# Performance work log

Hardware: AMD Instinct MI355X
Metric: run time of the kernel (lower is better)

## Reference

```python
import jax, jax.numpy as jnp
import numpy as np

N = 50000
E = 800000
D = 128          # feature_dimension
H = 2 * D        # hidden = 2*feature_dimension
C = 8            # num_edge_colours


def setup_inputs() -> dict:
    key = jax.random.key(0)
    ks = jax.random.split(key, 9)
    x = jax.random.normal(ks[0], (N, D), dtype=jnp.float32)
    edge_index = jax.random.randint(ks[1], (2, E), 0, N, dtype=jnp.int64)
    edge_colour = jax.random.randint(ks[2], (E,), 0, C, dtype=jnp.int64)
    # conv weights init: normal(0, 0.001) as in the torch module
    W_conv1 = 0.001 * jax.random.normal(ks[3], (C, H, D), dtype=jnp.float32)
    W_conv2 = 0.001 * jax.random.normal(ks[4], (C, D, H), dtype=jnp.float32)
    # nn.Linear default init: U(-1/sqrt(fan_in), 1/sqrt(fan_in))
    b1 = 1.0 / np.sqrt(D)
    b2 = 1.0 / np.sqrt(H)
    W_self1 = jax.random.uniform(ks[5], (H, D), jnp.float32, -b1, b1)
    b_self1 = jax.random.uniform(ks[6], (H,), jnp.float32, -b1, b1)
    W_self2 = jax.random.uniform(ks[7], (D, H), jnp.float32, -b2, b2)
    b_self2 = jax.random.uniform(ks[8], (D,), jnp.float32, -b2, b2)
    return {
        "x": x, "edge_index": edge_index, "edge_colour": edge_colour,
        "W_self1": W_self1, "b_self1": b_self1,
        "W_self2": W_self2, "b_self2": b_self2,
        "W_conv1": W_conv1, "W_conv2": W_conv2,
    }


def _ec_conv(h, src, seg, Wc):
    # Per-colour gather -> scatter-add -> colour-specific linear, summed over colours.
    # seg = colour * N + dst combines (colour, dst) into one segment id so a single
    # segment_sum covers all colours (equivalent to the per-colour masked loops).
    msgs = h[src]                                             # [E, F]
    agg = jax.ops.segment_sum(msgs, seg, num_segments=C * N)  # [C*N, F]
    agg = agg.reshape(C, N, h.shape[1])                       # [C, N, F]
    return jnp.einsum('cnf,cof->no', agg, Wc)                 # [N, O]


def reference(x, edge_index, edge_colour, W_self1, b_self1, W_self2, b_self2,
              W_conv1, W_conv2):
    src = edge_index[0]   # message() uses x_j = x[src], aggregated at dst
    dst = edge_index[1]
    seg = edge_colour * N + dst
    h = x @ W_self1.T + b_self1 + _ec_conv(x, src, seg, W_conv1)
    h = jax.nn.relu(h)
    h2 = h @ W_self2.T + b_self2 + _ec_conv(h, src, seg, W_conv2)
    return jax.nn.sigmoid(h2 - 10.0)
```

## Files before the change

### kernel.cpp

```cpp
#include <hip/hip_runtime.h>


#define NN 50000
#define EE 800000
#define DD 128
#define HH 256
#define CC 8
#define K1 1152

typedef unsigned short u16;
typedef __attribute__((ext_vector_type(8))) short s16x8;
typedef __attribute__((ext_vector_type(4))) float f32x4;

__device__ __forceinline__ float bf2f(short u) {
  return __uint_as_float(((unsigned)(u16)u) << 16);
}
__device__ __forceinline__ u16 f2bf(float f) {
  unsigned u = __float_as_uint(f);
  u = (u + 0x7FFFu + ((u >> 16) & 1u)) >> 16;
  return (u16)u;
}


__global__ void k_castx(const float* __restrict__ x, u16* __restrict__ xb) {
  int i = blockIdx.x * 256 + threadIdx.x;
  if (i < NN * DD) xb[i] = f2bf(x[i]);
}

__global__ void k_wt1f(const float* __restrict__ Wc1, const float* __restrict__ Ws1,
                       u16* __restrict__ W) {
  int i = blockIdx.x * 256 + threadIdx.x;
  if (i >= 294912) return;
  int e = i & 7;
  int t = i >> 3;
  int rs = t & 15; t >>= 4;
  int kg = t & 3;  t >>= 2;
  int kk = t % 36;
  int col16 = t / 36;
  int col = col16 * 16 + rs;
  int k = kk * 32 + kg * 8 + e;
  float v = (k < CC * DD) ? Wc1[(k >> 7) * (HH * DD) + col * DD + (k & 127)]
                          : Ws1[col * DD + (k - CC * DD)];
  W[i] = f2bf(v);
}

__global__ void k_wt2f(const float* __restrict__ Wc2, const float* __restrict__ Ws2,
                       u16* __restrict__ W) {
  int i = blockIdx.x * 256 + threadIdx.x;
  if (i >= 294912) return;
  int e = i & 7;
  int t = i >> 3;
  int rs = t & 15; t >>= 4;
  int kg = t & 3;  t >>= 2;
  int kk = t & 7;
  int col16 = t >> 3;
  int oc = col16 * 16 + rs;
  int c = oc >> 7, o = oc & 127;
  int k = kk * 32 + kg * 8 + e;
  float v = (c < CC) ? Wc2[c * (DD * HH) + o * HH + k] : Ws2[o * HH + k];
  W[i] = f2bf(v);
}


__global__ void k_hist(const int* __restrict__ ei, const int* __restrict__ ec,
                       int* __restrict__ counts) {
  int e = blockIdx.x * 256 + threadIdx.x;
  if (e < EE) {
    int dst = ei[EE + e];
    int c = ec[e];
    atomicAdd(&counts[dst * CC + c], 1);
  }
}

__global__ void k_offsets(const int* __restrict__ counts, int2* __restrict__ oc,
                          int* __restrict__ cursor, int* __restrict__ gcount) {
  __shared__ int lds[256];
  __shared__ int basesh;
  int tid = threadIdx.x;
  int i = blockIdx.x * 256 + tid;
  int c = (i < CC * NN) ? counts[i] : 0;
  lds[tid] = c;
  __syncthreads();
  int v = c;
  for (int s = 1; s < 256; s <<= 1) {
    int t = (tid >= s) ? lds[tid - s] : 0;
    __syncthreads();
    v += t;
    lds[tid] = v;
    __syncthreads();
  }
  if (tid == 255) basesh = atomicAdd(gcount, v);
  __syncthreads();
  int excl = basesh + v - c;
  if (i < CC * NN) {
    oc[i] = make_int2(excl, c);
    cursor[i] = excl;
  }
}

__global__ void k_fill(const int* __restrict__ ei, const int* __restrict__ ec,
                       int* __restrict__ cursor, int* __restrict__ sv) {
  int e = blockIdx.x * 256 + threadIdx.x;
  if (e < EE) {
    int src = ei[e];
    int dst = ei[EE + e];
    int c = ec[e];
    int slot = atomicAdd(&cursor[dst * CC + c], 1);
    sv[slot] = src * 8 + c;
  }
}


__global__ void __launch_bounds__(256) k_agg1(
    const u16* __restrict__ xb, const int2* __restrict__ oc,
    const int* __restrict__ sv, u16* __restrict__ agg) {
  int item = blockIdx.x * 256 + threadIdx.x;
  int dst = item >> 4, ch = item & 15;
  int eoff = ch * 8;
#pragma unroll
  for (int c = 0; c < CC; ++c) {
    int2 se = oc[dst * CC + c];
    float s[8];
#pragma unroll
    for (int q = 0; q < 8; q++) s[q] = 0.f;
    int j = 0;
    for (; j + 1 < se.y; j += 2) {
      int s0 = sv[se.x + j] >> 3;
      int s1 = sv[se.x + j + 1] >> 3;
      s16x8 v0 = *(const s16x8*)(xb + (size_t)s0 * DD + eoff);
      s16x8 v1 = *(const s16x8*)(xb + (size_t)s1 * DD + eoff);
#pragma unroll
      for (int q = 0; q < 8; q++) s[q] += bf2f(v0[q]) + bf2f(v1[q]);
    }
    if (j < se.y) {
      int s0 = sv[se.x + j] >> 3;
      s16x8 v0 = *(const s16x8*)(xb + (size_t)s0 * DD + eoff);
#pragma unroll
      for (int q = 0; q < 8; q++) s[q] += bf2f(v0[q]);
    }
    s16x8 r;
#pragma unroll
    for (int q = 0; q < 8; q++) r[q] = (short)f2bf(s[q]);
    *(s16x8*)(agg + ((size_t)c * NN + dst) * DD + eoff) = r;
  }
}


#define LOADA(af, p) do {                                                      \
  if ((p) < CC) {                                                              \
    _Pragma("unroll") for (int rg = 0; rg < 2; ++rg)                           \
    _Pragma("unroll") for (int kk = 0; kk < 4; ++kk)                           \
      af[rg][kk] = *(const s16x8*)(agg + ((size_t)(p) * NN + rowA[rg]) * DD +  \
                                   kk * 32 + kg * 8);                          \
  } else {                                                                     \
    _Pragma("unroll") for (int rg = 0; rg < 2; ++rg)                           \
    _Pragma("unroll") for (int kk = 0; kk < 4; ++kk)                           \
      af[rg][kk] = *(const s16x8*)(xb + (size_t)rowA[rg] * DD +                \
                                   kk * 32 + kg * 8);                          \
  } } while (0)

#define STAGE1(p, buf) do {                                                    \
  _Pragma("unroll") for (int i = 0; i < 8; ++i) {                              \
    const u16* gsrc = Wf + (size_t)((ch * 8 + i) * 36 + (p) * 4 + w) * 512 +   \
                      lane * 8;                                                \
    u16* lptr = Bs + (buf) * 16384 + (i * 4 + w) * 512;                        \
    __builtin_amdgcn_global_load_lds(                                          \
        (const __attribute__((address_space(1))) void*)gsrc,                   \
        (__attribute__((address_space(3))) void*)lptr, 16, 0, 0);              \
  } } while (0)

#define MFMAPH(af, buf) do {                                                   \
  _Pragma("unroll") for (int kk = 0; kk < 4; ++kk)                             \
  _Pragma("unroll") for (int fc = 0; fc < 8; ++fc) {                           \
    s16x8 bfr = *(const s16x8*)(Bs + (buf) * 16384 + (fc * 4 + kk) * 512 +     \
                                lane * 8);                                     \
    _Pragma("unroll") for (int rg = 0; rg < 2; ++rg)                           \
      acc[rg][fc] = __builtin_amdgcn_mfma_f32_16x16x32_bf16(af[rg][kk], bfr,   \
                                                            acc[rg][fc], 0, 0, 0); \
  } } while (0)

__global__ void __launch_bounds__(256, 1) k_gemm1s(
    const u16* __restrict__ xb, const u16* __restrict__ agg,
    const u16* __restrict__ Wf, const float* __restrict__ b1,
    u16* __restrict__ hb) {
  __shared__ u16 Bs[32768];
  int ch = blockIdx.x;
  int rb = blockIdx.y;
  int tid = threadIdx.x;
  int w = tid >> 6, lane = tid & 63;
  int rs = lane & 15, kg = lane >> 4;
  int r0 = rb * 128 + w * 32;

  int rowA[2];
#pragma unroll
  for (int rg = 0; rg < 2; ++rg) rowA[rg] = min(r0 + rg * 16 + rs, NN - 1);

  f32x4 acc[2][8];
#pragma unroll
  for (int rg = 0; rg < 2; ++rg)
#pragma unroll
    for (int i = 0; i < 8; i++)
#pragma unroll
      for (int q = 0; q < 4; q++) acc[rg][i][q] = 0.f;

  s16x8 afA[2][4], afB[2][4];
  STAGE1(0, 0);
  LOADA(afA, 0);
  __syncthreads();

#pragma unroll
  for (int ph = 0; ph < 9; ++ph) {
    const int pb = ph & 1;
    if (ph < 8) {
      STAGE1(ph + 1, pb ^ 1);
      if (pb == 0) { LOADA(afB, ph + 1); } else { LOADA(afA, ph + 1); }
    }
    if (pb == 0) { MFMAPH(afA, 0); } else { MFMAPH(afB, 1); }
    __syncthreads();
  }

#pragma unroll
  for (int fc = 0; fc < 8; ++fc) {
    int col = ch * 128 + fc * 16 + rs;
    float bias = b1[col];
#pragma unroll
    for (int rg = 0; rg < 2; ++rg) {
#pragma unroll
      for (int q = 0; q < 4; ++q) {
        float v = acc[rg][fc][q] + bias;
        if (v < 0.f) v = 0.f;
        int rr = r0 + rg * 16 + kg * 4 + q;
        if (rr < NN) hb[(size_t)rr * HH + col] = f2bf(v);
      }
    }
  }
}


__global__ void __launch_bounds__(256, 3) k_gemm2g(
    const u16* __restrict__ hb, const u16* __restrict__ Wf,
    u16* __restrict__ g2) {
  __shared__ u16 Bs[24576];
  int cb = blockIdx.x;
  int rb = blockIdx.y;
  int tid = threadIdx.x;
  int w = tid >> 6, lane = tid & 63;
  int rs = lane & 15, kg = lane >> 4;
  int c16b = cb * 6;

  {
    const u16* src = Wf + (size_t)cb * 24576;
#pragma unroll
    for (int i = 0; i < 12; ++i) {
      int o = (i * 256 + tid) * 8;
      *(s16x8*)(Bs + o) = *(const s16x8*)(src + o);
    }
  }
  __syncthreads();

#pragma unroll
  for (int tt = 0; tt < 2; ++tt) {
    int t = w + tt * 4;
    int r0 = rb * 256 + t * 32;
    int rowA[2];
#pragma unroll
    for (int rg = 0; rg < 2; ++rg) rowA[rg] = min(r0 + rg * 16 + rs, NN - 1);

    s16x8 af[2][8];
#pragma unroll
    for (int rg = 0; rg < 2; ++rg)
#pragma unroll
      for (int kk = 0; kk < 8; ++kk)
        af[rg][kk] = *(const s16x8*)(hb + (size_t)rowA[rg] * HH + kk * 32 + kg * 8);

    f32x4 acc[2][6];
#pragma unroll
    for (int rg = 0; rg < 2; ++rg)
#pragma unroll
      for (int i = 0; i < 6; i++)
#pragma unroll
        for (int q = 0; q < 4; q++) acc[rg][i][q] = 0.f;

#pragma unroll
    for (int kk = 0; kk < 8; ++kk) {
#pragma unroll
      for (int fc = 0; fc < 6; ++fc) {
        s16x8 bfr = *(const s16x8*)(Bs + ((fc * 8 + kk) * 64 + lane) * 8);
#pragma unroll
        for (int rg = 0; rg < 2; ++rg)
          acc[rg][fc] = __builtin_amdgcn_mfma_f32_16x16x32_bf16(af[rg][kk], bfr, acc[rg][fc], 0, 0, 0);
      }
    }

#pragma unroll
    for (int rg = 0; rg < 2; ++rg) {
#pragma unroll
      for (int q = 0; q < 4; ++q) {
        int rr = r0 + rg * 16 + kg * 4 + q;
        if (rr < NN) {
#pragma unroll
          for (int fc = 0; fc < 6; ++fc) {
            int col = (c16b + fc) * 16 + rs;
            g2[(size_t)rr * 1152 + col] = f2bf(acc[rg][fc][q]);
          }
        }
      }
    }
  }
}


__global__ void __launch_bounds__(256) k_final(
    const u16* __restrict__ g2, const float* __restrict__ b2,
    const int2* __restrict__ oc, const int* __restrict__ sv,
    float* __restrict__ out) {
  int item = blockIdx.x * 256 + threadIdx.x;
  if (item >= NN * 8) return;
  int dst = item >> 3, ch = item & 7;
  int eoff = ch * 16;

  int st, cn;
  {
    int2 a0 = oc[dst * CC];
    int2 a7 = oc[dst * CC + 7];
    st = a0.x;
    cn = a7.x + a7.y - a0.x;
  }

  float s[16];
  {
    const u16* sp = g2 + (size_t)dst * 1152 + 1024 + eoff;
    s16x8 lo = *(const s16x8*)sp;
    s16x8 hi = *(const s16x8*)(sp + 8);
#pragma unroll
    for (int q = 0; q < 8; q++) s[q] = b2[eoff + q] + bf2f(lo[q]);
#pragma unroll
    for (int q = 0; q < 8; q++) s[q + 8] = b2[eoff + 8 + q] + bf2f(hi[q]);
  }

  for (int j = 0; j < cn; j += 4) {
    int pofs[4];
#pragma unroll
    for (int t = 0; t < 4; t++) {
      int jj = j + t;
      if (jj < cn) {
        int v = sv[st + jj];
        pofs[t] = (v >> 3) * 1152 + (v & 7) * 128;
      } else {
        pofs[t] = -1;
      }
    }
#pragma unroll
    for (int t = 0; t < 4; t++) {
      if (pofs[t] >= 0) {
        const u16* pp = g2 + pofs[t] + eoff;
        s16x8 lo = *(const s16x8*)pp;
        s16x8 hi = *(const s16x8*)(pp + 8);
#pragma unroll
        for (int q = 0; q < 8; q++) s[q] += bf2f(lo[q]);
#pragma unroll
        for (int q = 0; q < 8; q++) s[q + 8] += bf2f(hi[q]);
      }
    }
  }
  float* op = out + (size_t)dst * DD + eoff;
#pragma unroll
  for (int q = 0; q < 16; q++) op[q] = 1.f / (1.f + expf(10.f - s[q]));
}


extern "C" void kernel_launch(void* const* d_in, const int* in_sizes, int n_in,
                              void* d_out, int out_size, void* d_ws, size_t ws_size,
                              hipStream_t stream) {
  const float* x   = (const float*)d_in[0];
  const int*   ei  = (const int*)d_in[1];
  const int*   ec  = (const int*)d_in[2];
  const float* Ws1 = (const float*)d_in[3];
  const float* b1  = (const float*)d_in[4];
  const float* Ws2 = (const float*)d_in[5];
  const float* b2  = (const float*)d_in[6];
  const float* Wc1 = (const float*)d_in[7];
  const float* Wc2 = (const float*)d_in[8];
  float* out = (float*)d_out;

  char* p = (char*)d_ws;
  u16*  g2     = (u16*)p;
  u16*  agg1   = (u16*)p;
  u16*  xb     = (u16*)(p + 102400000);
  u16*  hb     = (u16*)(p + 115200000);
  u16*  W1f    = (u16*)(p + 140800000);
  u16*  W2f    = (u16*)(p + 141389824);
  int2* oc     = (int2*)(p + 141979648);
  int*  sv     = (int*)(p + 145179648);
  int*  counts = (int*)(p + 148379648);
  int*  gcount = (int*)(p + 149979648);
  int*  cursor = (int*)(p + 149979904);

  hipMemsetAsync(counts, 0, 1600256, stream);

  k_castx<<<25000, 256, 0, stream>>>(x, xb);
  k_wt1f<<<1152, 256, 0, stream>>>(Wc1, Ws1, W1f);
  k_wt2f<<<1152, 256, 0, stream>>>(Wc2, Ws2, W2f);

  k_hist<<<3125, 256, 0, stream>>>(ei, ec, counts);
  k_offsets<<<1563, 256, 0, stream>>>(counts, oc, cursor, gcount);
  k_fill<<<3125, 256, 0, stream>>>(ei, ec, cursor, sv);

  k_agg1<<<3125, 256, 0, stream>>>(xb, oc, sv, agg1);
  k_gemm1s<<<dim3(2, 391), 256, 0, stream>>>(xb, agg1, W1f, b1, hb);
  k_gemm2g<<<dim3(12, 196), 256, 0, stream>>>(hb, W2f, g2);
  k_final<<<1563, 256, 0, stream>>>(g2, b2, oc, sv, out);
}
```

Measured before the change: 350.2 us.

## Store layer-1 aggregates and conv weights in FP8 and use FP8 MFMA

The per-colour aggregates from k_agg1 are now written as FP8 (e4m3) instead of bf16. The layer-1 conv weights are pre-scaled by 256 and packed to FP8, and the first GEMM runs its eight colour phases with the fp8 MFMA, rescaling before a final bf16 phase for the self-weight term. This halves the aggregate write and read traffic and the weight staging bytes, and uses the higher-rate fp8 matrix instructions. It also vectorises the x-to-bf16 cast. The cost is reduced precision on aggregates and weights, with some risk to accuracy.

```diff
diff --git a/kernel.cpp b/kernel.cpp
--- a/kernel.cpp
+++ b/kernel.cpp
@@ -6,9 +6,10 @@
 #define DD 128
 #define HH 256
 #define CC 8
-#define K1 1152
 
 typedef unsigned short u16;
+typedef unsigned char u8;
+typedef unsigned long long u64;
 typedef __attribute__((ext_vector_type(8))) short s16x8;
 typedef __attribute__((ext_vector_type(4))) float f32x4;
 
@@ -24,24 +25,42 @@
 
 __global__ void k_castx(const float* __restrict__ x, u16* __restrict__ xb) {
   int i = blockIdx.x * 256 + threadIdx.x;
-  if (i < NN * DD) xb[i] = f2bf(x[i]);
-}
-
-__global__ void k_wt1f(const float* __restrict__ Wc1, const float* __restrict__ Ws1,
-                       u16* __restrict__ W) {
+  const float4* xp = (const float4*)x + (size_t)i * 2;
+  float4 a = xp[0], b = xp[1];
+  s16x8 r;
+  r[0] = f2bf(a.x); r[1] = f2bf(a.y); r[2] = f2bf(a.z); r[3] = f2bf(a.w);
+  r[4] = f2bf(b.x); r[5] = f2bf(b.y); r[6] = f2bf(b.z); r[7] = f2bf(b.w);
+  *(s16x8*)(xb + (size_t)i * 8) = r;
+}
+
+__global__ void k_wt1c8(const float* __restrict__ Wc1, unsigned* __restrict__ W) {
+  int t = blockIdx.x * 256 + threadIdx.x;
+  if (t >= 65536) return;
+  int half = t & 1;
+  int slot = t >> 1;
+  int lane = slot & 63;
+  int sk = slot >> 6;
+  int kkg = sk & 31, col16 = sk >> 5;
+  int col = col16 * 16 + (lane & 15);
+  int kb = kkg * 32 + (lane >> 4) * 8 + half * 4;
+  int c = kb >> 7, f = kb & 127;
+  const float* wp = Wc1 + (size_t)c * (HH * DD) + col * DD + f;
+  unsigned r = __builtin_amdgcn_cvt_pk_fp8_f32(wp[0] * 256.f, wp[1] * 256.f, 0, false);
+  r = __builtin_amdgcn_cvt_pk_fp8_f32(wp[2] * 256.f, wp[3] * 256.f, r, true);
+  W[t] = r;
+}
+
+__global__ void k_wt1s(const float* __restrict__ Ws1, u16* __restrict__ W) {
   int i = blockIdx.x * 256 + threadIdx.x;
-  if (i >= 294912) return;
+  if (i >= 32768) return;
   int e = i & 7;
-  int t = i >> 3;
-  int rs = t & 15; t >>= 4;
-  int kg = t & 3;  t >>= 2;
-  int kk = t % 36;
-  int col16 = t / 36;
-  int col = col16 * 16 + rs;
-  int k = kk * 32 + kg * 8 + e;
-  float v = (k < CC * DD) ? Wc1[(k >> 7) * (HH * DD) + col * DD + (k & 127)]
-                          : Ws1[col * DD + (k - CC * DD)];
-  W[i] = f2bf(v);
+  int slot = i >> 3;
+  int lane = slot & 63;
+  int sk = slot >> 6;
+  int kk = sk & 3, col16 = sk >> 2;
+  int col = col16 * 16 + (lane & 15);
+  int k = kk * 32 + (lane >> 4) * 8 + e;
+  W[i] = f2bf(Ws1[col * DD + k]);
 }
 
 __global__ void k_wt2f(const float* __restrict__ Wc2, const float* __restrict__ Ws2,
@@ -113,7 +132,7 @@
 
 __global__ void __launch_bounds__(256) k_agg1(
     const u16* __restrict__ xb, const int2* __restrict__ oc,
-    const int* __restrict__ sv, u16* __restrict__ agg) {
+    const int* __restrict__ sv, u8* __restrict__ aggf8) {
   int item = blockIdx.x * 256 + threadIdx.x;
   int dst = item >> 4, ch = item & 15;
   int eoff = ch * 8;
@@ -138,52 +157,75 @@
 #pragma unroll
       for (int q = 0; q < 8; q++) s[q] += bf2f(v0[q]);
     }
-    s16x8 r;
-#pragma unroll
-    for (int q = 0; q < 8; q++) r[q] = (short)f2bf(s[q]);
-    *(s16x8*)(agg + ((size_t)c * NN + dst) * DD + eoff) = r;
-  }
-}
-
-
-#define LOADA(af, p) do {                                                      \
-  if ((p) < CC) {                                                              \
-    _Pragma("unroll") for (int rg = 0; rg < 2; ++rg)                           \
-    _Pragma("unroll") for (int kk = 0; kk < 4; ++kk)                           \
-      af[rg][kk] = *(const s16x8*)(agg + ((size_t)(p) * NN + rowA[rg]) * DD +  \
-                                   kk * 32 + kg * 8);                          \
-  } else {                                                                     \
-    _Pragma("unroll") for (int rg = 0; rg < 2; ++rg)                           \
-    _Pragma("unroll") for (int kk = 0; kk < 4; ++kk)                           \
-      af[rg][kk] = *(const s16x8*)(xb + (size_t)rowA[rg] * DD +                \
-                                   kk * 32 + kg * 8);                          \
+    unsigned r0 = __builtin_amdgcn_cvt_pk_fp8_f32(s[0], s[1], 0, false);
+    r0 = __builtin_amdgcn_cvt_pk_fp8_f32(s[2], s[3], r0, true);
+    unsigned r1 = __builtin_amdgcn_cvt_pk_fp8_f32(s[4], s[5], 0, false);
+    r1 = __builtin_amdgcn_cvt_pk_fp8_f32(s[6], s[7], r1, true);
+    *(uint2*)(aggf8 + ((size_t)c * NN + dst) * 128 + eoff) = make_uint2(r0, r1);
+  }
+}
+
+
+#define LOADA8(af, p) do {                                                     \
+  _Pragma("unroll") for (int rg = 0; rg < 2; ++rg)                             \
+  _Pragma("unroll") for (int kk = 0; kk < 4; ++kk)                             \
+    af[rg][kk] = *(const u64*)(aggf8 + ((size_t)(p) * NN + rowA[rg]) * 128 +   \
+                               kk * 32 + kg * 8);                              \
+  } while (0)
+
+#define LOADAS(af) do {                                                        \
+  _Pragma("unroll") for (int rg = 0; rg < 2; ++rg)                             \
+  _Pragma("unroll") for (int kk = 0; kk < 4; ++kk)                             \
+    af[rg][kk] = *(const s16x8*)(xb + (size_t)rowA[rg] * DD + kk * 32 + kg * 8); \
+  } while (0)
+
+#define STAGE8(p, buf) do {                                                    \
+  _Pragma("unroll") for (int i2 = 0; i2 < 4; ++i2) {                           \
+    int fc = i2 * 2 + (w >> 1);                                                \
+    int kb2 = (w & 1) * 2;                                                     \
+    const char* gs = (const char*)W1c8 +                                       \
+        (((ch * 8 + fc) * 32 + (p) * 4 + kb2) << 9) + lane * 16;               \
+    char* lp = Bs + (buf) * 32768 + ((fc * 4 + kb2) << 9);                     \
+    __builtin_amdgcn_global_load_lds(                                          \
+        (const __attribute__((address_space(1))) void*)gs,                     \
+        (__attribute__((address_space(3))) void*)lp, 16, 0, 0);                \
   } } while (0)
 
-#define STAGE1(p, buf) do {                                                    \
-  _Pragma("unroll") for (int i = 0; i < 8; ++i) {                              \
-    const u16* gsrc = Wf + (size_t)((ch * 8 + i) * 36 + (p) * 4 + w) * 512 +   \
-                      lane * 8;                                                \
-    u16* lptr = Bs + (buf) * 16384 + (i * 4 + w) * 512;                        \
+#define STAGES(buf) do {                                                       \
+  _Pragma("unroll") for (int i2 = 0; i2 < 8; ++i2) {                           \
+    const char* gs = (const char*)W1s + (((ch * 8 + i2) * 4 + w) << 10) +      \
+                     lane * 16;                                                \
+    char* lp = Bs + (buf) * 32768 + ((i2 * 4 + w) << 10);                      \
     __builtin_amdgcn_global_load_lds(                                          \
-        (const __attribute__((address_space(1))) void*)gsrc,                   \
-        (__attribute__((address_space(3))) void*)lptr, 16, 0, 0);              \
+        (const __attribute__((address_space(1))) void*)gs,                     \
+        (__attribute__((address_space(3))) void*)lp, 16, 0, 0);                \
   } } while (0)
 
-#define MFMAPH(af, buf) do {                                                   \
+#define MFMA8(af, buf) do {                                                    \
   _Pragma("unroll") for (int kk = 0; kk < 4; ++kk)                             \
   _Pragma("unroll") for (int fc = 0; fc < 8; ++fc) {                           \
-    s16x8 bfr = *(const s16x8*)(Bs + (buf) * 16384 + (fc * 4 + kk) * 512 +     \
-                                lane * 8);                                     \
+    long bfr = *(const long*)(Bs + (buf) * 32768 + ((fc * 4 + kk) << 9) +      \
+                              lane * 8);                                       \
+    _Pragma("unroll") for (int rg = 0; rg < 2; ++rg)                           \
+      acc[rg][fc] = __builtin_amdgcn_mfma_f32_16x16x32_fp8_fp8(                \
+          (long)af[rg][kk], bfr, acc[rg][fc], 0, 0, 0);                        \
+  } } while (0)
+
+#define MFMAS(af, buf) do {                                                    \
+  _Pragma("unroll") for (int kk = 0; kk < 4; ++kk)                             \
+  _Pragma("unroll") for (int fc = 0; fc < 8; ++fc) {                           \
+    s16x8 bfr = *(const s16x8*)(Bs + (buf) * 32768 + ((fc * 4 + kk) << 10) +   \
+                                lane * 16);                                    \
     _Pragma("unroll") for (int rg = 0; rg < 2; ++rg)                           \
       acc[rg][fc] = __builtin_amdgcn_mfma_f32_16x16x32_bf16(af[rg][kk], bfr,   \
                                                             acc[rg][fc], 0, 0, 0); \
   } } while (0)
 
 __global__ void __launch_bounds__(256, 1) k_gemm1s(
-    const u16* __restrict__ xb, const u16* __restrict__ agg,
-    const u16* __restrict__ Wf, const float* __restrict__ b1,
-    u16* __restrict__ hb) {
-  __shared__ u16 Bs[32768];
+    const u16* __restrict__ xb, const u8* __restrict__ aggf8,
+    const unsigned* __restrict__ W1c8, const u16* __restrict__ W1s,
+    const float* __restrict__ b1, u16* __restrict__ hb) {
+  __shared__ char Bs[65536];
   int ch = blockIdx.x;
   int rb = blockIdx.y;
   int tid = threadIdx.x;
@@ -203,21 +245,32 @@
 #pragma unroll
       for (int q = 0; q < 4; q++) acc[rg][i][q] = 0.f;
 
-  s16x8 afA[2][4], afB[2][4];
-  STAGE1(0, 0);
-  LOADA(afA, 0);
+  u64 af8A[2][4], af8B[2][4];
+  s16x8 afS[2][4];
+  STAGE8(0, 0);
+  LOADA8(af8A, 0);
   __syncthreads();
 
 #pragma unroll
-  for (int ph = 0; ph < 9; ++ph) {
-    const int pb = ph & 1;
-    if (ph < 8) {
-      STAGE1(ph + 1, pb ^ 1);
-      if (pb == 0) { LOADA(afB, ph + 1); } else { LOADA(afA, ph + 1); }
-    }
-    if (pb == 0) { MFMAPH(afA, 0); } else { MFMAPH(afB, 1); }
+  for (int ph = 0; ph < 8; ++ph) {
+    const int cb = ph & 1, nb = cb ^ 1;
+    if (ph < 7) {
+      STAGE8(ph + 1, nb);
+      if (cb == 0) { LOADA8(af8B, ph + 1); } else { LOADA8(af8A, ph + 1); }
+    } else {
+      STAGES(nb);
+      LOADAS(afS);
+    }
+    if (cb == 0) { MFMA8(af8A, 0); } else { MFMA8(af8B, 1); }
     __syncthreads();
   }
+#pragma unroll
+  for (int rg = 0; rg < 2; ++rg)
+#pragma unroll
+    for (int i = 0; i < 8; i++)
+#pragma unroll
+      for (int q = 0; q < 4; q++) acc[rg][i][q] *= 0.00390625f;
+  MFMAS(afS, 0);
 
 #pragma unroll
   for (int fc = 0; fc < 8; ++fc) {
@@ -385,29 +438,31 @@
 
   char* p = (char*)d_ws;
   u16*  g2     = (u16*)p;
-  u16*  agg1   = (u16*)p;
-  u16*  xb     = (u16*)(p + 102400000);
-  u16*  hb     = (u16*)(p + 115200000);
-  u16*  W1f    = (u16*)(p + 140800000);
-  u16*  W2f    = (u16*)(p + 141389824);
-  int2* oc     = (int2*)(p + 141979648);
-  int*  sv     = (int*)(p + 145179648);
-  int*  counts = (int*)(p + 148379648);
-  int*  gcount = (int*)(p + 149979648);
-  int*  cursor = (int*)(p + 149979904);
+  u8*   aggf8  = (u8*)p;
+  u16*  xb     = (u16*)(p + 115200000);
+  u16*  hb     = (u16*)(p + 128000000);
+  unsigned* W1c8 = (unsigned*)(p + 153600000);
+  u16*  W1s    = (u16*)(p + 153862144);
+  u16*  W2f    = (u16*)(p + 153927680);
+  int2* oc     = (int2*)(p + 154517504);
+  int*  sv     = (int*)(p + 157717504);
+  int*  counts = (int*)(p + 160917504);
+  int*  gcount = (int*)(p + 162517504);
+  int*  cursor = (int*)(p + 162517760);
 
   hipMemsetAsync(counts, 0, 1600256, stream);
 
-  k_castx<<<25000, 256, 0, stream>>>(x, xb);
-  k_wt1f<<<1152, 256, 0, stream>>>(Wc1, Ws1, W1f);
+  k_castx<<<3125, 256, 0, stream>>>(x, xb);
+  k_wt1c8<<<256, 256, 0, stream>>>(Wc1, W1c8);
+  k_wt1s<<<128, 256, 0, stream>>>(Ws1, W1s);
   k_wt2f<<<1152, 256, 0, stream>>>(Wc2, Ws2, W2f);
 
   k_hist<<<3125, 256, 0, stream>>>(ei, ec, counts);
   k_offsets<<<1563, 256, 0, stream>>>(counts, oc, cursor, gcount);
   k_fill<<<3125, 256, 0, stream>>>(ei, ec, cursor, sv);
 
-  k_agg1<<<3125, 256, 0, stream>>>(xb, oc, sv, agg1);
-  k_gemm1s<<<dim3(2, 391), 256, 0, stream>>>(xb, agg1, W1f, b1, hb);
+  k_agg1<<<3125, 256, 0, stream>>>(xb, oc, sv, aggf8);
+  k_gemm1s<<<dim3(2, 391), 256, 0, stream>>>(xb, aggf8, W1c8, W1s, b1, hb);
   k_gemm2g<<<dim3(12, 196), 256, 0, stream>>>(hb, W2f, g2);
   k_final<<<1563, 256, 0, stream>>>(g2, b2, oc, sv, out);
 }
```

Result: faster. 330.1 us (-5.8%).
